# Kernel tuning notes

Hardware: AMD Instinct MI355X
Metric: run time of the kernel (lower is better)

The kernel has to match this reference:

```python
import jax, jax.numpy as jnp
import numpy as np
from jax import lax

K = 7            # pool_size / PSROI_BINS
C_OUT = 10       # output channels per bin (features has K*K*C_OUT channels)
FEAT_STRIDE = 16
LAMDA = 0.1
SAMPLES = 2      # bilinear sample points per bin side
H = W = 200
C_IN = K * K * C_OUT  # 490
N_ROIS = 512


def setup_inputs() -> dict:
    key = jax.random.key(0)
    k1, k2, k3, k4 = jax.random.split(key, 4)
    features = jax.random.normal(k1, (1, H, W, C_IN), jnp.float32)
    conv_w = jax.random.truncated_normal(k2, -2.0, 2.0, (3, 3, C_IN, 2 * K * K), jnp.float32) * 0.01
    img = H * FEAT_STRIDE  # image-space extent
    cxy = jax.random.uniform(k3, (N_ROIS, 2), minval=0.0, maxval=img - 1.0)
    wh = jax.random.uniform(k4, (N_ROIS, 2), minval=64.0, maxval=640.0)
    x1 = jnp.clip(cxy[:, 0] - wh[:, 0] * 0.5, 0.0, img - 2.0)
    y1 = jnp.clip(cxy[:, 1] - wh[:, 1] * 0.5, 0.0, img - 2.0)
    x2 = jnp.clip(x1 + wh[:, 0], x1 + 1.0, img - 1.0)
    y2 = jnp.clip(y1 + wh[:, 1], y1 + 1.0, img - 1.0)
    rois = jnp.stack([jnp.zeros(N_ROIS), x1, y1, x2, y2], axis=-1)  # [N,5]
    return {"features": features, "rois": rois, "conv_w": conv_w}


def _bilinear(feat, y, x):
    """feat [H,W,C]; y,x arbitrary equal shapes -> [..., C]."""
    Hf, Wf = feat.shape[0], feat.shape[1]
    y = jnp.clip(y, 0.0, Hf - 1.0)
    x = jnp.clip(x, 0.0, Wf - 1.0)
    y0 = jnp.floor(y)
    x0 = jnp.floor(x)
    y0i = y0.astype(jnp.int32)
    x0i = x0.astype(jnp.int32)
    y1i = jnp.minimum(y0i + 1, Hf - 1)
    x1i = jnp.minimum(x0i + 1, Wf - 1)
    wy = (y - y0)[..., None]
    wx = (x - x0)[..., None]
    v00 = feat[y0i, x0i]
    v01 = feat[y0i, x1i]
    v10 = feat[y1i, x0i]
    v11 = feat[y1i, x1i]
    return (v00 * (1 - wy) * (1 - wx) + v01 * (1 - wy) * wx
            + v10 * wy * (1 - wx) + v11 * wy * wx)


def _ps_roi(feat, box, cpg, offsets):
    """Position-sensitive RoI avg pooling with optional per-bin offsets.
    feat [H,W,K*K*cpg]; box (x1,y1,x2,y2) image coords; offsets [K,K,2] (dx,dy)
    in image coords or None. Returns [K,K,cpg]."""
    x1, y1, x2, y2 = box
    fx1 = x1 / FEAT_STRIDE
    fy1 = y1 / FEAT_STRIDE
    bw = (x2 - x1 + 1.0) / FEAT_STRIDE / K
    bh = (y2 - y1 + 1.0) / FEAT_STRIDE / K
    idx = jnp.arange(K, dtype=feat.dtype)
    s = (jnp.arange(SAMPLES, dtype=feat.dtype) + 0.5) / SAMPLES
    sx = fx1 + (idx[:, None] + s[None, :]) * bw  # [K(j), S]
    sy = fy1 + (idx[:, None] + s[None, :]) * bh  # [K(i), S]
    gx = jnp.broadcast_to(sx[None, :, None, :], (K, K, SAMPLES, SAMPLES))
    gy = jnp.broadcast_to(sy[:, None, :, None], (K, K, SAMPLES, SAMPLES))
    if offsets is not None:
        off = offsets / FEAT_STRIDE  # image -> feature coords
        gx = gx + off[..., 0][:, :, None, None]
        gy = gy + off[..., 1][:, :, None, None]
    vals = _bilinear(feat, gy, gx)                     # [K,K,S,S,K*K*cpg]
    vals = vals.reshape(K, K, SAMPLES, SAMPLES, K * K, cpg)
    bin_idx = (jnp.arange(K)[:, None] * K + jnp.arange(K)[None, :])  # [K,K]
    sel = jnp.take_along_axis(
        vals, bin_idx[:, :, None, None, None, None], axis=4)[..., 0, :]
    return sel.mean(axis=(2, 3))  # [K,K,cpg]


def reference(features, rois, conv_w):
    # 3x3 same conv producing 2*K*K offset channels (no bias)
    offset_map = lax.conv_general_dilated(
        features, conv_w, (1, 1), 'SAME',
        dimension_numbers=('NHWC', 'HWIO', 'NHWC'))[0]  # [H,W,2*K*K]
    feat0 = features[0]  # [H,W,K*K*C_OUT]

    def one_roi(roi):
        x1, y1, x2, y2 = roi[1], roi[2], roi[3], roi[4]
        rw = x2 - x1 + 1.0
        rh = y2 - y1 + 1.0
        box = (x1, y1, x2, y2)
        # stage 1: pool the offset map position-sensitively -> [K,K,2]
        off = _ps_roi(offset_map, box, 2, None).reshape(-1, 2)
        off = jnp.stack((off[:, 0] * rw * LAMDA,
                         off[:, 1] * rh * LAMDA), axis=-1).reshape(K, K, 2)
        # stage 2: deformable PS-RoI pooling of the features -> [K,K,C_OUT]
        return _ps_roi(feat0, box, C_OUT, off)

    return jax.vmap(one_roi)(rois)  # [N, K, K, C_OUT]
```

## Files before the change

kernel.cpp:

```cpp
#include <hip/hip_runtime.h>
#include <hip/hip_bf16.h>

#define Hh   200
#define Ww   200
#define CIN  490
#define OCN  98
#define KK   7
#define COUT 10
#define NROIS 512
#define PIX  8

#define PH   202
#define PW   202
#define PC   512
#define NPIX (Hh * Ww)
#define KCN  16
#define NF   7
#define NUNITS 144
#define NGRAN  36

typedef __attribute__((ext_vector_type(8))) short short8;
typedef __attribute__((ext_vector_type(4))) float float4v;

__global__ __launch_bounds__(256) void pack_feat_kernel(
    const float* __restrict__ feat, __hip_bfloat16* __restrict__ pf)
{
    int tid = blockIdx.x * 256 + threadIdx.x;
    if (tid >= PH * PW * (PC / 8)) return;
    int c8  = (tid & 63) * 8;
    int pix = tid >> 6;
    int py = pix / PW, px = pix % PW;
    __hip_bfloat16* dst = pf + (size_t)pix * PC + c8;
    bool interior = (py >= 1 && py <= Hh && px >= 1 && px <= Ww);

    __hip_bfloat16 v[8];
    if (interior && c8 + 8 <= CIN) {
        const float* s = feat + ((size_t)(py - 1) * Ww + (px - 1)) * CIN + c8;
#pragma unroll
        for (int q = 0; q < 4; ++q) {
            float2 f2 = *reinterpret_cast<const float2*>(s + q * 2);
            v[q * 2]     = __float2bfloat16(f2.x);
            v[q * 2 + 1] = __float2bfloat16(f2.y);
        }
    } else {
        const float* s = interior ? feat + ((size_t)(py - 1) * Ww + (px - 1)) * CIN : nullptr;
#pragma unroll
        for (int j = 0; j < 8; ++j) {
            float val = (interior && (c8 + j) < CIN) ? s[c8 + j] : 0.f;
            v[j] = __float2bfloat16(val);
        }
    }
    *reinterpret_cast<short8*>(dst) = *reinterpret_cast<short8*>(v);
}

__global__ __launch_bounds__(256) void pack_w_kernel(
    const float* __restrict__ w, __hip_bfloat16* __restrict__ bp)
{
    int idx = blockIdx.x * 256 + threadIdx.x;
    if (idx >= NUNITS * NF * 64 * 8) return;
    int j = idx & 7;
    int l = (idx >> 3) & 63;
    int f = (idx >> 9) % NF;
    int u = idx / (NF * 512);
    int kc = u / 9, tap = u % 9;
    int k = kc * 32 + ((l >> 4) * 8) + j;
    int n = f * 16 + (l & 15);
    float val = (k < CIN && n < OCN) ? w[((size_t)tap * CIN + k) * OCN + n] : 0.f;
    bp[idx] = __float2bfloat16(val);
}

__global__ __launch_bounds__(640) void conv_mfma_kernel(
    const short* __restrict__ pf,
    const short* __restrict__ bp,
    float* __restrict__ om)
{
    __shared__ short bsm[8 * 3584];

    int orig = blockIdx.x;
    int xcd = orig & 7;
    int pos = orig >> 3;
    int blk = ((xcd < 2) ? xcd * 32 : 64 + (xcd - 2) * 31) + pos;

    int l = threadIdx.x & 63;
    int w = threadIdx.x >> 6;
    int m0 = blk * 160 + w * 16;

    int row = m0 + (l & 15);
    int y = row / Ww, x = row % Ww;
    const short* abase = pf + ((size_t)(y * PW + x) * PC) + ((l >> 4) * 8);

    float4v acc[NF];
#pragma unroll
    for (int f = 0; f < NF; ++f) acc[f] = (float4v){0.f, 0.f, 0.f, 0.f};

    auto aOff = [&](int u) -> int {
        int kc = u / 9, tap = u - kc * 9;
        int ky = tap / 3, kx = tap - ky * 3;
        return (ky * PW + kx) * PC + kc * 32;
    };

#pragma unroll
    for (int s = 0; s < 3; ++s) {
        int i = w + s * 10;
        if (i < 28) {
            int u = i / 7, f = i % 7;
            short8 v = *reinterpret_cast<const short8*>(
                bp + ((size_t)(u * NF + f)) * 512 + l * 8);
            *reinterpret_cast<short8*>(&bsm[(u & 7) * 3584 + f * 512 + l * 8]) = v;
        }
    }
    short8 a0 = *reinterpret_cast<const short8*>(abase + aOff(0));
    short8 a1 = *reinterpret_cast<const short8*>(abase + aOff(1));
    short8 a2 = *reinterpret_cast<const short8*>(abase + aOff(2));
    short8 a3 = *reinterpret_cast<const short8*>(abase + aOff(3));
    __syncthreads();

    for (int g = 0; g < NGRAN; ++g) {
        bool more = (g < NGRAN - 1);
        int u0n = (g + 1) * 4;

        short8 st0, st1, st2;
        int off0 = -1, off1 = -1, off2 = -1;
        if (more) {
            {
                int i = w;
                int uu = u0n + i / 7, f = i % 7;
                st0 = *reinterpret_cast<const short8*>(
                    bp + ((size_t)(uu * NF + f)) * 512 + l * 8);
                off0 = (uu & 7) * 3584 + f * 512 + l * 8;
            }
            {
                int i = w + 10;
                int uu = u0n + i / 7, f = i % 7;
                st1 = *reinterpret_cast<const short8*>(
                    bp + ((size_t)(uu * NF + f)) * 512 + l * 8);
                off1 = (uu & 7) * 3584 + f * 512 + l * 8;
            }
            if (w + 20 < 28) {
                int i = w + 20;
                int uu = u0n + i / 7, f = i % 7;
                st2 = *reinterpret_cast<const short8*>(
                    bp + ((size_t)(uu * NF + f)) * 512 + l * 8);
                off2 = (uu & 7) * 3584 + f * 512 + l * 8;
            }
        }
        short8 n0, n1, n2, n3;
        if (more) {
            n0 = *reinterpret_cast<const short8*>(abase + aOff(u0n + 0));
            n1 = *reinterpret_cast<const short8*>(abase + aOff(u0n + 1));
            n2 = *reinterpret_cast<const short8*>(abase + aOff(u0n + 2));
            n3 = *reinterpret_cast<const short8*>(abase + aOff(u0n + 3));
        }

        int u0 = g * 4;
#define COMPUTE_UNIT(J, AREG)                                                   \
        {                                                                       \
            int sbase = ((u0 + J) & 7) * 3584 + l * 8;                          \
            _Pragma("unroll")                                                   \
            for (int f = 0; f < NF; ++f) {                                      \
                short8 b = *reinterpret_cast<short8*>(&bsm[sbase + f * 512]);   \
                acc[f] = __builtin_amdgcn_mfma_f32_16x16x32_bf16(               \
                    AREG, b, acc[f], 0, 0, 0);                                  \
            }                                                                   \
        }
        COMPUTE_UNIT(0, a0)
        COMPUTE_UNIT(1, a1)
        COMPUTE_UNIT(2, a2)
        COMPUTE_UNIT(3, a3)
#undef COMPUTE_UNIT

        if (off0 >= 0) *reinterpret_cast<short8*>(&bsm[off0]) = st0;
        if (off1 >= 0) *reinterpret_cast<short8*>(&bsm[off1]) = st1;
        if (off2 >= 0) *reinterpret_cast<short8*>(&bsm[off2]) = st2;
        if (more) { a0 = n0; a1 = n1; a2 = n2; a3 = n3; }
        __syncthreads();
    }

    int n = l & 15;
    int rbase = m0 + ((l >> 4) * 4);
#pragma unroll
    for (int f = 0; f < NF; ++f) {
        int col = f * 16 + n;
        if (col < OCN) {
#pragma unroll
            for (int j = 0; j < 4; ++j)
                om[(size_t)(rbase + j) * OCN + col] = acc[f][j];
        }
    }
}

__global__ __launch_bounds__(256) void conv3x3_kernel(
    const float* __restrict__ feat, const float* __restrict__ w,
    const float* __restrict__ zero, float* __restrict__ om)
{
    int idx = blockIdx.x * blockDim.x + threadIdx.x;
    if (idx >= Hh * (Ww / PIX) * OCN) return;
    int oc = idx % OCN;
    int g  = idx / OCN;
    int x0 = (g % (Ww / PIX)) * PIX;
    int y  = g / (Ww / PIX);

    float acc[PIX];
#pragma unroll
    for (int p = 0; p < PIX; ++p) acc[p] = 0.f;

    for (int ky = 0; ky < 3; ++ky) {
        int yy = y + ky - 1;
        if (yy < 0 || yy >= Hh) continue;
        const float* frow = feat + (size_t)yy * Ww * CIN;
        for (int kx = 0; kx < 3; ++kx) {
            const float* wp = w + ((ky * 3 + kx) * CIN) * OCN + oc;
            const float* fp[PIX];
#pragma unroll
            for (int p = 0; p < PIX; ++p) {
                int xx = x0 + p + kx - 1;
                fp[p] = (xx >= 0 && xx < Ww) ? (frow + (size_t)xx * CIN) : zero;
            }
            for (int ic = 0; ic < CIN; ic += 2) {
                float w0 = wp[ic * OCN];
                float w1 = wp[(ic + 1) * OCN];
#pragma unroll
                for (int p = 0; p < PIX; ++p) {
                    float2 f = *reinterpret_cast<const float2*>(fp[p] + ic);
                    acc[p] = fmaf(f.x, w0, acc[p]);
                    acc[p] = fmaf(f.y, w1, acc[p]);
                }
            }
        }
    }
    float* orow = om + ((size_t)y * Ww + x0) * OCN + oc;
#pragma unroll
    for (int p = 0; p < PIX; ++p) orow[p * OCN] = acc[p];
}

__device__ __forceinline__ void bilin_setup(float y, float x,
    int& i00, int& i01, int& i10, int& i11,
    float& w00, float& w01, float& w10, float& w11)
{
    y = fminf(fmaxf(y, 0.f), 199.f);
    x = fminf(fmaxf(x, 0.f), 199.f);
    float y0f = floorf(y), x0f = floorf(x);
    int y0 = (int)y0f, x0i = (int)x0f;
    int y1 = min(y0 + 1, 199), x1 = min(x0i + 1, 199);
    float wy = y - y0f, wx = x - x0f;
    i00 = y0 * Ww + x0i;  i01 = y0 * Ww + x1;
    i10 = y1 * Ww + x0i;  i11 = y1 * Ww + x1;
    w00 = (1.f - wy) * (1.f - wx);
    w01 = (1.f - wy) * wx;
    w10 = wy * (1.f - wx);
    w11 = wy * wx;
}

__global__ __launch_bounds__(256) void psroi_kernel(
    const float* __restrict__ feat, const float* __restrict__ rois,
    const float* __restrict__ om, float* __restrict__ out)
{
    int n = blockIdx.x;
    int t = threadIdx.x;

    float x1 = rois[n * 5 + 1], y1 = rois[n * 5 + 2];
    float x2 = rois[n * 5 + 3], y2 = rois[n * 5 + 4];
    float rw = x2 - x1 + 1.0f, rh = y2 - y1 + 1.0f;
    float fx1 = x1 * 0.0625f, fy1 = y1 * 0.0625f;
    float bw = (rw * 0.0625f) / 7.0f;
    float bh = (rh * 0.0625f) / 7.0f;

    __shared__ float offs[49][2];

    if (t < 49) {
        int bi = t / 7, bj = t % 7;
        float ax = 0.f, ay = 0.f;
#pragma unroll
        for (int ss = 0; ss < 4; ++ss) {
            float sj = ((float)(ss & 1) + 0.5f) * 0.5f;
            float si = ((float)(ss >> 1) + 0.5f) * 0.5f;
            float gx = fx1 + ((float)bj + sj) * bw;
            float gy = fy1 + ((float)bi + si) * bh;
            int i00, i01, i10, i11; float w00, w01, w10, w11;
            bilin_setup(gy, gx, i00, i01, i10, i11, w00, w01, w10, w11);
            int c0 = t * 2;
            const float* p00 = om + (size_t)i00 * OCN + c0;
            const float* p01 = om + (size_t)i01 * OCN + c0;
            const float* p10 = om + (size_t)i10 * OCN + c0;
            const float* p11 = om + (size_t)i11 * OCN + c0;
            ax += w00 * p00[0] + w01 * p01[0] + w10 * p10[0] + w11 * p11[0];
            ay += w00 * p00[1] + w01 * p01[1] + w10 * p10[1] + w11 * p11[1];
        }
        offs[t][0] = ax * 0.25f * rw * 0.1f * 0.0625f;
        offs[t][1] = ay * 0.25f * rh * 0.1f * 0.0625f;
    }
    __syncthreads();

    for (int o = t; o < KK * KK * COUT; o += blockDim.x) {
        int bin = o / COUT, c = o % COUT;
        int bi = bin / 7, bj = bin % 7;
        float dx = offs[bin][0], dy = offs[bin][1];
        int ch = bin * COUT + c;
        float acc = 0.f;
#pragma unroll
        for (int ss = 0; ss < 4; ++ss) {
            float sj = ((float)(ss & 1) + 0.5f) * 0.5f;
            float si = ((float)(ss >> 1) + 0.5f) * 0.5f;
            float gx = fx1 + ((float)bj + sj) * bw + dx;
            float gy = fy1 + ((float)bi + si) * bh + dy;
            int i00, i01, i10, i11; float w00, w01, w10, w11;
            bilin_setup(gy, gx, i00, i01, i10, i11, w00, w01, w10, w11);
            acc += w00 * feat[(size_t)i00 * CIN + ch]
                 + w01 * feat[(size_t)i01 * CIN + ch]
                 + w10 * feat[(size_t)i10 * CIN + ch]
                 + w11 * feat[(size_t)i11 * CIN + ch];
        }
        out[(size_t)n * (KK * KK * COUT) + o] = acc * 0.25f;
    }
}

extern "C" void kernel_launch(void* const* d_in, const int* in_sizes, int n_in,
                              void* d_out, int out_size, void* d_ws, size_t ws_size,
                              hipStream_t stream) {
    const float* feat = (const float*)d_in[0];
    const float* rois = (const float*)d_in[1];
    const float* w    = (const float*)d_in[2];
    float* out = (float*)d_out;

    const size_t OM_BYTES = (size_t)NPIX * OCN * 4;
    const size_t BP_BYTES = (size_t)NUNITS * NF * 64 * 8 * 2;
    const size_t PF_BYTES = (size_t)PH * PW * PC * 2;
    const size_t NEEDED = OM_BYTES + BP_BYTES + PF_BYTES;

    if (ws_size >= NEEDED) {
        float* om = (float*)d_ws;
        __hip_bfloat16* bp = (__hip_bfloat16*)((char*)d_ws + OM_BYTES);
        __hip_bfloat16* pf = (__hip_bfloat16*)((char*)d_ws + OM_BYTES + BP_BYTES);

        int wThreads = NUNITS * NF * 64 * 8;
        pack_w_kernel<<<(wThreads + 255) / 256, 256, 0, stream>>>(w, bp);
        int fThreads = PH * PW * (PC / 8);
        pack_feat_kernel<<<(fThreads + 255) / 256, 256, 0, stream>>>(feat, pf);
        conv_mfma_kernel<<<250, 640, 0, stream>>>(
            (const short*)pf, (const short*)bp, om);
        psroi_kernel<<<NROIS, 256, 0, stream>>>(feat, rois, om, out);
    } else {
        float* zero = (float*)d_ws;
        float* om   = (float*)d_ws + 1024;
        hipMemsetAsync(d_ws, 0, 4096, stream);
        int convThreads = Hh * (Ww / PIX) * OCN;
        conv3x3_kernel<<<(convThreads + 255) / 256, 256, 0, stream>>>(feat, w, zero, om);
        psroi_kernel<<<NROIS, 256, 0, stream>>>(feat, rois, om, out);
    }
}
```

Measured before the change: 93.19 us.

## Switch offset conv to 32x32x16 MFMA tiles with N split across waves

```diff
diff --git a/kernel.cpp b/kernel.cpp
--- a/kernel.cpp
+++ b/kernel.cpp
@@ -14,13 +14,13 @@
 #define PW   202
 #define PC   512
 #define NPIX (Hh * Ww)
-#define KCN  16
-#define NF   7
-#define NUNITS 144
-#define NGRAN  36
+#define NT   4
+#define NU32 288
+#define NG32 72
 
 typedef __attribute__((ext_vector_type(8))) short short8;
 typedef __attribute__((ext_vector_type(4))) float float4v;
+typedef __attribute__((ext_vector_type(16))) float float16v;
 
 __global__ __launch_bounds__(256) void pack_feat_kernel(
     const float* __restrict__ feat, __hip_bfloat16* __restrict__ pf)
@@ -57,14 +57,14 @@
     const float* __restrict__ w, __hip_bfloat16* __restrict__ bp)
 {
     int idx = blockIdx.x * 256 + threadIdx.x;
-    if (idx >= NUNITS * NF * 64 * 8) return;
+    if (idx >= NU32 * NT * 64 * 8) return;
     int j = idx & 7;
     int l = (idx >> 3) & 63;
-    int f = (idx >> 9) % NF;
-    int u = idx / (NF * 512);
+    int t = (idx >> 9) & 3;
+    int u = idx >> 11;
     int kc = u / 9, tap = u % 9;
-    int k = kc * 32 + ((l >> 4) * 8) + j;
-    int n = f * 16 + (l & 15);
+    int k = kc * 16 + ((l >> 5) * 8) + j;
+    int n = t * 32 + (l & 31);
     float val = (k < CIN && n < OCN) ? w[((size_t)tap * CIN + k) * OCN + n] : 0.f;
     bp[idx] = __float2bfloat16(val);
 }
@@ -74,39 +74,34 @@
     const short* __restrict__ bp,
     float* __restrict__ om)
 {
-    __shared__ short bsm[8 * 3584];
-
-    int orig = blockIdx.x;
-    int xcd = orig & 7;
-    int pos = orig >> 3;
-    int blk = ((xcd < 2) ? xcd * 32 : 64 + (xcd - 2) * 31) + pos;
+    __shared__ short bsm[8 * 2048];
 
     int l = threadIdx.x & 63;
     int w = threadIdx.x >> 6;
-    int m0 = blk * 160 + w * 16;
-
-    int row = m0 + (l & 15);
+    int nh = w & 1;
+    int m0 = blockIdx.x * 160 + (w >> 1) * 32;
+
+    int row = m0 + (l & 31);
     int y = row / Ww, x = row % Ww;
-    const short* abase = pf + ((size_t)(y * PW + x) * PC) + ((l >> 4) * 8);
-
-    float4v acc[NF];
-#pragma unroll
-    for (int f = 0; f < NF; ++f) acc[f] = (float4v){0.f, 0.f, 0.f, 0.f};
+    const short* abase = pf + ((size_t)(y * PW + x) * PC) + ((l >> 5) * 8);
+
+    float16v acc0 = {0.f,0.f,0.f,0.f,0.f,0.f,0.f,0.f,0.f,0.f,0.f,0.f,0.f,0.f,0.f,0.f};
+    float16v acc1 = {0.f,0.f,0.f,0.f,0.f,0.f,0.f,0.f,0.f,0.f,0.f,0.f,0.f,0.f,0.f,0.f};
 
     auto aOff = [&](int u) -> int {
         int kc = u / 9, tap = u - kc * 9;
         int ky = tap / 3, kx = tap - ky * 3;
-        return (ky * PW + kx) * PC + kc * 32;
+        return (ky * PW + kx) * PC + kc * 16;
     };
 
 #pragma unroll
-    for (int s = 0; s < 3; ++s) {
+    for (int s = 0; s < 2; ++s) {
         int i = w + s * 10;
-        if (i < 28) {
-            int u = i / 7, f = i % 7;
+        if (i < 16) {
+            int uu = i >> 2, t = i & 3;
             short8 v = *reinterpret_cast<const short8*>(
-                bp + ((size_t)(u * NF + f)) * 512 + l * 8);
-            *reinterpret_cast<short8*>(&bsm[(u & 7) * 3584 + f * 512 + l * 8]) = v;
+                bp + ((size_t)(uu * NT + t)) * 512 + l * 8);
+            *reinterpret_cast<short8*>(&bsm[(uu & 7) * 2048 + t * 512 + l * 8]) = v;
         }
     }
     short8 a0 = *reinterpret_cast<const short8*>(abase + aOff(0));
@@ -115,33 +110,26 @@
     short8 a3 = *reinterpret_cast<const short8*>(abase + aOff(3));
     __syncthreads();
 
-    for (int g = 0; g < NGRAN; ++g) {
-        bool more = (g < NGRAN - 1);
+    for (int g = 0; g < NG32; ++g) {
+        bool more = (g < NG32 - 1);
         int u0n = (g + 1) * 4;
 
-        short8 st0, st1, st2;
-        int off0 = -1, off1 = -1, off2 = -1;
+        short8 st0, st1;
+        int off0 = -1, off1 = -1;
         if (more) {
             {
                 int i = w;
-                int uu = u0n + i / 7, f = i % 7;
+                int uu = u0n + (i >> 2), t = i & 3;
                 st0 = *reinterpret_cast<const short8*>(
-                    bp + ((size_t)(uu * NF + f)) * 512 + l * 8);
-                off0 = (uu & 7) * 3584 + f * 512 + l * 8;
-            }
-            {
+                    bp + ((size_t)(uu * NT + t)) * 512 + l * 8);
+                off0 = (uu & 7) * 2048 + t * 512 + l * 8;
+            }
+            if (w + 10 < 16) {
                 int i = w + 10;
-                int uu = u0n + i / 7, f = i % 7;
+                int uu = u0n + (i >> 2), t = i & 3;
                 st1 = *reinterpret_cast<const short8*>(
-                    bp + ((size_t)(uu * NF + f)) * 512 + l * 8);
-                off1 = (uu & 7) * 3584 + f * 512 + l * 8;
-            }
-            if (w + 20 < 28) {
-                int i = w + 20;
-                int uu = u0n + i / 7, f = i % 7;
-                st2 = *reinterpret_cast<const short8*>(
-                    bp + ((size_t)(uu * NF + f)) * 512 + l * 8);
-                off2 = (uu & 7) * 3584 + f * 512 + l * 8;
+                    bp + ((size_t)(uu * NT + t)) * 512 + l * 8);
+                off1 = (uu & 7) * 2048 + t * 512 + l * 8;
             }
         }
         short8 n0, n1, n2, n3;
@@ -155,13 +143,11 @@
         int u0 = g * 4;
 #define COMPUTE_UNIT(J, AREG)                                                   \
         {                                                                       \
-            int sbase = ((u0 + J) & 7) * 3584 + l * 8;                          \
-            _Pragma("unroll")                                                   \
-            for (int f = 0; f < NF; ++f) {                                      \
-                short8 b = *reinterpret_cast<short8*>(&bsm[sbase + f * 512]);   \
-                acc[f] = __builtin_amdgcn_mfma_f32_16x16x32_bf16(               \
-                    AREG, b, acc[f], 0, 0, 0);                                  \
-            }                                                                   \
+            int sbase = ((u0 + J) & 7) * 2048 + nh * 1024 + l * 8;              \
+            short8 b0 = *reinterpret_cast<short8*>(&bsm[sbase]);                \
+            short8 b1 = *reinterpret_cast<short8*>(&bsm[sbase + 512]);          \
+            acc0 = __builtin_amdgcn_mfma_f32_32x32x16_bf16(AREG, b0, acc0, 0, 0, 0); \
+            acc1 = __builtin_amdgcn_mfma_f32_32x32x16_bf16(AREG, b1, acc1, 0, 0, 0); \
         }
         COMPUTE_UNIT(0, a0)
         COMPUTE_UNIT(1, a1)
@@ -171,20 +157,22 @@
 
         if (off0 >= 0) *reinterpret_cast<short8*>(&bsm[off0]) = st0;
         if (off1 >= 0) *reinterpret_cast<short8*>(&bsm[off1]) = st1;
-        if (off2 >= 0) *reinterpret_cast<short8*>(&bsm[off2]) = st2;
         if (more) { a0 = n0; a1 = n1; a2 = n2; a3 = n3; }
         __syncthreads();
     }
 
-    int n = l & 15;
-    int rbase = m0 + ((l >> 4) * 4);
-#pragma unroll
-    for (int f = 0; f < NF; ++f) {
-        int col = f * 16 + n;
+    int col_lo = l & 31;
+    int rbase = m0 + 4 * (l >> 5);
+#pragma unroll
+    for (int tt = 0; tt < 2; ++tt) {
+        int col = (nh * 2 + tt) * 32 + col_lo;
         if (col < OCN) {
-#pragma unroll
-            for (int j = 0; j < 4; ++j)
-                om[(size_t)(rbase + j) * OCN + col] = acc[f][j];
+            const float16v& A = tt ? acc1 : acc0;
+#pragma unroll
+            for (int reg = 0; reg < 16; ++reg) {
+                int r = rbase + (reg & 3) + 8 * (reg >> 2);
+                om[(size_t)r * OCN + col] = A[reg];
+            }
         }
     }
 }
@@ -323,7 +311,7 @@
     float* out = (float*)d_out;
 
     const size_t OM_BYTES = (size_t)NPIX * OCN * 4;
-    const size_t BP_BYTES = (size_t)NUNITS * NF * 64 * 8 * 2;
+    const size_t BP_BYTES = (size_t)NU32 * NT * 64 * 8 * 2;
     const size_t PF_BYTES = (size_t)PH * PW * PC * 2;
     const size_t NEEDED = OM_BYTES + BP_BYTES + PF_BYTES;
 
@@ -332,7 +320,7 @@
         __hip_bfloat16* bp = (__hip_bfloat16*)((char*)d_ws + OM_BYTES);
         __hip_bfloat16* pf = (__hip_bfloat16*)((char*)d_ws + OM_BYTES + BP_BYTES);
 
-        int wThreads = NUNITS * NF * 64 * 8;
+        int wThreads = NU32 * NT * 64 * 8;
         pack_w_kernel<<<(wThreads + 255) / 256, 256, 0, stream>>>(w, bp);
         int fThreads = PH * PW * (PC / 8);
         pack_feat_kernel<<<(fThreads + 255) / 256, 256, 0, stream>>>(feat, pf);
```

Result: slower. 134.2 us (+44.1%).
